# Optimization experiments

Measured on AMD Instinct MI355X. Metric: run time of the kernel, lower is better.

Reference implementation:

```python
import jax, jax.numpy as jnp
import numpy as np

N_NODES = 4096
N_EDGES = 100000
N_PAIRS = 1000000
MAX_PATH = 5
EDGE_DIM = 16


def setup_inputs() -> dict:
    key = jax.random.key(0)
    k1, k2, k3, k4, k5, k6 = jax.random.split(key, 6)
    x = jax.random.normal(k1, (N_NODES, EDGE_DIM), dtype=jnp.float32)
    edge_attr = jax.random.normal(k2, (N_EDGES, EDGE_DIM), dtype=jnp.float32)
    edge_vector = jax.random.normal(k3, (MAX_PATH, EDGE_DIM), dtype=jnp.float32)
    # unique (src, dst) pairs so the scatter-set is well-defined (matches the
    # dict-of-dicts edge_paths, where each (src, dst) appears at most once)
    pair_ids = jax.random.permutation(k4, N_NODES * N_NODES)[:N_PAIRS]
    src_idx = (pair_ids // N_NODES).astype(jnp.int64)
    dst_idx = (pair_ids % N_NODES).astype(jnp.int64)
    # ragged paths: random length in [1, MAX_PATH], padded with -1
    path_idx = jax.random.randint(k5, (N_PAIRS, MAX_PATH), 0, N_EDGES).astype(jnp.int64)
    lengths = jax.random.randint(k6, (N_PAIRS, 1), 1, MAX_PATH + 1)
    valid = jnp.arange(MAX_PATH)[None, :] < lengths
    path_idx = jnp.where(valid, path_idx, -1)
    return {"x": x, "edge_attr": edge_attr, "edge_vector": edge_vector,
            "src_idx": src_idx, "dst_idx": dst_idx, "path_idx": path_idx}


def reference(x, edge_attr, edge_vector, src_idx, dst_idx, path_idx):
    # path_idx: [P, L] edge indices, -1 = padding beyond the path length
    n = x.shape[0]
    mask = path_idx >= 0                                   # [P, L]
    safe = jnp.where(mask, path_idx, 0)
    feats = edge_attr[safe]                                # [P, L, D] irregular gather
    dots = jnp.einsum('pld,ld->pl', feats, edge_vector)    # per-hop dot products
    dots = jnp.where(mask, dots, 0.0)
    cnt = mask.sum(axis=-1)                                # path lengths
    # mean over the path; empty path -> 0 (matches nan_to_num on 0/0)
    vals = jnp.where(cnt > 0, dots.sum(axis=-1) / jnp.maximum(cnt, 1).astype(dots.dtype), 0.0)
    cij = jnp.zeros((n, n), dtype=x.dtype).at[src_idx, dst_idx].set(vals)
    return cij
```

## Files before the change

### kernel.cpp

```cpp
#include <hip/hip_runtime.h>

#define N_NODES  4096
#define MAX_PATH 5
#define EDGE_DIM 16

typedef int   iv2 __attribute__((ext_vector_type(2)));
typedef float fv2 __attribute__((ext_vector_type(2)));

__global__ __launch_bounds__(256) void precompute_dots_kernel(
    const float* __restrict__ edge_attr,
    const float* __restrict__ edge_vector,
    float*       __restrict__ D,
    int n_edges)
{
    int e = blockIdx.x * blockDim.x + threadIdx.x;
    if (e >= n_edges) return;

    const float4* ea = (const float4*)(edge_attr + (size_t)e * EDGE_DIM);
    float4 a0 = ea[0], a1 = ea[1], a2 = ea[2], a3 = ea[3];

#pragma unroll
    for (int l = 0; l < MAX_PATH; ++l) {
        const float4* ev = (const float4*)(edge_vector + l * EDGE_DIM);
        float4 b0 = ev[0], b1 = ev[1], b2 = ev[2], b3 = ev[3];
        float d = a0.x*b0.x + a0.y*b0.y + a0.z*b0.z + a0.w*b0.w
                + a1.x*b1.x + a1.y*b1.y + a1.z*b1.z + a1.w*b1.w
                + a2.x*b2.x + a2.y*b2.y + a2.z*b2.z + a2.w*b2.w
                + a3.x*b3.x + a3.y*b3.y + a3.z*b3.z + a3.w*b3.w;
        D[(size_t)l * n_edges + e] = d;
    }
}

__global__ __launch_bounds__(256) void gather_vals_kernel(
    const float* __restrict__ D,
    const int*   __restrict__ path_idx,
    float*       __restrict__ vals,
    int n_pairs, int n_edges)
{
    int t  = blockIdx.x * blockDim.x + threadIdx.x;
    int p0 = t * 2;
    if (p0 >= n_pairs) return;

    const iv2* pp = (const iv2*)(path_idx + (size_t)p0 * MAX_PATH);
    iv2 w0 = pp[0], w1 = pp[1], w2 = pp[2], w3 = pp[3], w4 = pp[4];
    int e[10] = { w0.x, w0.y, w1.x, w1.y, w2.x,
                  w2.y, w3.x, w3.y, w4.x, w4.y };

    float g[10];
#pragma unroll
    for (int j = 0; j < 2; ++j) {
#pragma unroll
        for (int l = 0; l < MAX_PATH; ++l) {
            int idx = e[j * MAX_PATH + l];
            g[j * MAX_PATH + l] = (idx >= 0) ? D[(size_t)l * n_edges + idx] : 0.0f;
        }
    }

    fv2 v;
#pragma unroll
    for (int j = 0; j < 2; ++j) {
        float sum = 0.0f;
        int   cnt = 0;
#pragma unroll
        for (int l = 0; l < MAX_PATH; ++l) {
            if (e[j * MAX_PATH + l] >= 0) { sum += g[j * MAX_PATH + l]; ++cnt; }
        }
        v[j] = (cnt > 0) ? (sum / (float)cnt) : 0.0f;
    }
    *(fv2*)(vals + p0) = v;
}

__global__ __launch_bounds__(256) void scatter_vals_kernel(
    const float* __restrict__ vals,
    const int*   __restrict__ src_idx,
    const int*   __restrict__ dst_idx,
    float*       __restrict__ out,
    int n_pairs)
{
    int t  = blockIdx.x * blockDim.x + threadIdx.x;
    int p0 = t * 4;
    if (p0 >= n_pairs) return;

    if (p0 + 3 < n_pairs) {
        float4 v  = *(const float4*)(vals + p0);
        int4   sv = *(const int4*)(src_idx + p0);
        int4   dv = *(const int4*)(dst_idx + p0);
        out[(size_t)sv.x * N_NODES + dv.x] = v.x;
        out[(size_t)sv.y * N_NODES + dv.y] = v.y;
        out[(size_t)sv.z * N_NODES + dv.z] = v.z;
        out[(size_t)sv.w * N_NODES + dv.w] = v.w;
    } else {
        for (int p = p0; p < n_pairs; ++p)
            out[(size_t)src_idx[p] * N_NODES + dst_idx[p]] = vals[p];
    }
}

extern "C" void kernel_launch(void* const* d_in, const int* in_sizes, int n_in,
                              void* d_out, int out_size, void* d_ws, size_t ws_size,
                              hipStream_t stream)
{
    const float* edge_attr   = (const float*)d_in[1];
    const float* edge_vector = (const float*)d_in[2];
    const int*   src_idx     = (const int*)d_in[3];
    const int*   dst_idx     = (const int*)d_in[4];
    const int*   path_idx    = (const int*)d_in[5];
    float*       out         = (float*)d_out;

    const int n_edges = in_sizes[1] / EDGE_DIM;
    const int n_pairs = in_sizes[3];

    float* D    = (float*)d_ws;
    float* vals = (float*)((char*)d_ws + ((size_t)5 * n_edges * sizeof(float) + 1023 & ~(size_t)1023));

    hipMemsetAsync(d_out, 0, (size_t)out_size * sizeof(float), stream);

    const int block = 256;
    precompute_dots_kernel<<<(n_edges + block - 1) / block, block, 0, stream>>>(
        edge_attr, edge_vector, D, n_edges);

    const int tA = (n_pairs + 1) / 2;
    gather_vals_kernel<<<(tA + block - 1) / block, block, 0, stream>>>(
        D, path_idx, vals, n_pairs, n_edges);

    const int tB = (n_pairs + 3) / 4;
    scatter_vals_kernel<<<(tB + block - 1) / block, block, 0, stream>>>(
        vals, src_idx, dst_idx, out, n_pairs);
}
```

Baseline: 51.75 us.

## Fuse output zeroing into gather kernel with dedicated zeroing blocks

Replaces the separate hipMemsetAsync of the 64 MB output with 2048 extra blocks in the gather kernel that zero the output using nontemporal vector stores. The zeroing then runs concurrently with the latency-bound path gathers instead of serially before them, and one launch/memset op is removed. The risk is that the zeroing blocks compete with the gather blocks for bandwidth and slots, and the output size is hardcoded to N_NODES*N_NODES.

After: 61.55 us. +18.9%, slower.

```diff
diff --git a/kernel.cpp b/kernel.cpp
--- a/kernel.cpp
+++ b/kernel.cpp
@@ -6,6 +6,10 @@
 
 typedef int   iv2 __attribute__((ext_vector_type(2)));
 typedef float fv2 __attribute__((ext_vector_type(2)));
+typedef float fv4 __attribute__((ext_vector_type(4)));
+
+#define ZERO_BLOCKS 2048
+#define BLOCK 256
 
 __global__ __launch_bounds__(256) void precompute_dots_kernel(
     const float* __restrict__ edge_attr,
@@ -31,13 +35,24 @@
     }
 }
 
-__global__ __launch_bounds__(256) void gather_vals_kernel(
+__global__ __launch_bounds__(256) void zero_and_gather_kernel(
     const float* __restrict__ D,
     const int*   __restrict__ path_idx,
     float*       __restrict__ vals,
+    float*       __restrict__ out,
     int n_pairs, int n_edges)
 {
-    int t  = blockIdx.x * blockDim.x + threadIdx.x;
+    if ((int)blockIdx.x < ZERO_BLOCKS) {
+        const size_t nvec   = (size_t)N_NODES * N_NODES / 4;
+        const size_t stride = (size_t)ZERO_BLOCKS * BLOCK;
+        fv4 z = {0.f, 0.f, 0.f, 0.f};
+        fv4* o4 = (fv4*)out;
+        for (size_t i = (size_t)blockIdx.x * BLOCK + threadIdx.x; i < nvec; i += stride)
+            __builtin_nontemporal_store(z, o4 + i);
+        return;
+    }
+
+    int t  = ((int)blockIdx.x - ZERO_BLOCKS) * BLOCK + threadIdx.x;
     int p0 = t * 2;
     if (p0 >= n_pairs) return;
 
@@ -110,19 +125,17 @@
     const int n_pairs = in_sizes[3];
 
     float* D    = (float*)d_ws;
-    float* vals = (float*)((char*)d_ws + ((size_t)5 * n_edges * sizeof(float) + 1023 & ~(size_t)1023));
+    float* vals = (float*)((char*)d_ws +
+                  (((size_t)5 * n_edges * sizeof(float) + 1023) & ~(size_t)1023));
 
-    hipMemsetAsync(d_out, 0, (size_t)out_size * sizeof(float), stream);
-
-    const int block = 256;
-    precompute_dots_kernel<<<(n_edges + block - 1) / block, block, 0, stream>>>(
+    precompute_dots_kernel<<<(n_edges + BLOCK - 1) / BLOCK, BLOCK, 0, stream>>>(
         edge_attr, edge_vector, D, n_edges);
 
-    const int tA = (n_pairs + 1) / 2;
-    gather_vals_kernel<<<(tA + block - 1) / block, block, 0, stream>>>(
-        D, path_idx, vals, n_pairs, n_edges);
+    const int gather_blocks = ((n_pairs + 1) / 2 + BLOCK - 1) / BLOCK;
+    zero_and_gather_kernel<<<ZERO_BLOCKS + gather_blocks, BLOCK, 0, stream>>>(
+        D, path_idx, vals, out, n_pairs, n_edges);
 
     const int tB = (n_pairs + 3) / 4;
-    scatter_vals_kernel<<<(tB + block - 1) / block, block, 0, stream>>>(
+    scatter_vals_kernel<<<(tB + BLOCK - 1) / BLOCK, BLOCK, 0, stream>>>(
         vals, src_idx, dst_idx, out, n_pairs);
 }
```
